# Optimization experiments

Measured on AMD Instinct MI355X. Metric: run time of the kernel, lower is better.

Reference implementation:

```python
import jax, jax.numpy as jnp
import numpy as np

DELTA_VAR = 0.5
DELTA_DIST = 1.5
LOSS_WEIGHT = 1.0
L_MAX = 17  # segment ids 0..16 (0 = background)
EPS = 1e-12


def setup_inputs() -> dict:
    key = jax.random.key(0)
    k1, k2 = jax.random.split(key)
    B, D, H, W = 16, 16, 288, 512
    emb = jax.random.normal(k1, (B, D, H, W), dtype=jnp.float32)
    seg = jax.random.randint(k2, (B, 1, H, W), 0, L_MAX, dtype=jnp.int64)
    return {"input": emb, "target": seg}


def _per_image_losses(e, s):
    # e: [D, N] float, s: [N] int labels in [0, L_MAX)
    D, N = e.shape
    et = e.T  # [N, D]
    cnt = jax.ops.segment_sum(jnp.ones((N,), e.dtype), s, num_segments=L_MAX)  # [L]
    sums = jax.ops.segment_sum(et, s, num_segments=L_MAX)                      # [L, D]
    present = (cnt > 0) & (jnp.arange(L_MAX) != 0)
    num_lanes = jnp.sum(present).astype(e.dtype)
    means = sums / jnp.maximum(cnt, 1.0)[:, None]                              # [L, D]

    # variance (pull) term: per-pixel distance to own-label centroid
    diff = et - means[s]                                                       # [N, D]
    nrm = jnp.sqrt(jnp.maximum(jnp.sum(diff * diff, axis=1), EPS))             # [N]
    term = jax.nn.relu(nrm - DELTA_VAR) ** 2
    per_label = jax.ops.segment_sum(term, s, num_segments=L_MAX) / jnp.maximum(cnt, 1.0)
    var_l = jnp.sum(jnp.where(present, per_label, 0.0)) / jnp.maximum(num_lanes, 1.0)
    var_l = jnp.where(num_lanes > 0, var_l, 0.0)

    # distance (push) term: pairwise centroid distances among present lanes
    d = means[:, None, :] - means[None, :, :]                                  # [L, L, D]
    sumsq = jnp.sum(d * d, axis=2)                                             # [L, L]
    pair_mask = present[:, None] & present[None, :] & ~jnp.eye(L_MAX, dtype=bool)
    dist = jnp.sqrt(jnp.where(pair_mask, sumsq, 1.0))
    push = jnp.sum(jnp.where(pair_mask, jax.nn.relu(DELTA_DIST - dist) ** 2, 0.0))
    denom = jnp.maximum(num_lanes * (num_lanes - 1.0), 1.0)
    dist_l = jnp.where(num_lanes > 1, push / denom / 2.0, 0.0)
    return var_l, dist_l


def reference(input, target):
    B, D, H, W = input.shape
    N = H * W
    emb = input.reshape(B, D, N)
    seg = target.reshape(B, N).astype(jnp.int32)
    var_l, dist_l = jax.vmap(_per_image_losses)(emb, seg)
    loss = (jnp.sum(var_l) + jnp.sum(dist_l)) / B
    return loss * LOSS_WEIGHT
```

## Files before the change

### kernel.cpp

```cpp
#include <hip/hip_runtime.h>

#define BB   16
#define DD   16
#define NN   (288*512)
#define LL   17
#define TPB  256
#define NREP 16

#define PB   48
#define QB   (NN/4/PB)
#define PBV  144

#define FSCALE 32768.0f
#define INV_FSCALE (1.0f/32768.0f)
#define MW_STRIDE 320


__global__ __launch_bounds__(TPB) void k_accum(const float* __restrict__ emb,
                                               const int* __restrict__ seg,
                                               int* __restrict__ part) {
    __shared__ int tab[NREP * 289];
    const int tid  = threadIdx.x;
    const int b    = blockIdx.y;
    const int blk  = blockIdx.x;
    const int dgrp = tid >> 6;
    const int j    = tid & 63;
    int* trep = tab + (j & (NREP - 1)) * 289;

    for (int i = tid; i < NREP * 289; i += TPB) tab[i] = 0;

    const float* embb = emb + (size_t)b * DD * NN;
    const int*   segb = seg + (size_t)b * NN;
    const float* r0 = embb + (size_t)(dgrp * 4 + 0) * NN;
    const float* r1 = embb + (size_t)(dgrp * 4 + 1) * NN;
    const float* r2 = embb + (size_t)(dgrp * 4 + 2) * NN;
    const float* r3 = embb + (size_t)(dgrp * 4 + 3) * NN;
    const int q0 = blk * QB;
    __syncthreads();

    int n = (q0 + j) * 4;
    int4   s4 = *(const int4*)(segb + n);
    float4 e0 = *(const float4*)(r0 + n);
    float4 e1 = *(const float4*)(r1 + n);
    float4 e2 = *(const float4*)(r2 + n);
    float4 e3 = *(const float4*)(r3 + n);

#pragma unroll
    for (int it = 0; it < QB / 64; ++it) {
        int4 s4n; float4 e0n, e1n, e2n, e3n;
        if (it + 1 < QB / 64) {
            const int nn_ = (q0 + (it + 1) * 64 + j) * 4;
            s4n = *(const int4*)(segb + nn_);
            e0n = *(const float4*)(r0 + nn_);
            e1n = *(const float4*)(r1 + nn_);
            e2n = *(const float4*)(r2 + nn_);
            e3n = *(const float4*)(r3 + nn_);
        }
        const int ch = dgrp * 4;
        if (s4.x) {
            const int o0 = s4.x * 17 + ch;
            atomicAdd(trep + o0 + 0, __float2int_rn(e0.x * FSCALE));
            atomicAdd(trep + o0 + 1, __float2int_rn(e1.x * FSCALE));
            atomicAdd(trep + o0 + 2, __float2int_rn(e2.x * FSCALE));
            atomicAdd(trep + o0 + 3, __float2int_rn(e3.x * FSCALE));
            if (dgrp == 0) atomicAdd(trep + s4.x * 17 + 16, 1);
        }
        if (s4.y) {
            const int o1 = s4.y * 17 + ch;
            atomicAdd(trep + o1 + 0, __float2int_rn(e0.y * FSCALE));
            atomicAdd(trep + o1 + 1, __float2int_rn(e1.y * FSCALE));
            atomicAdd(trep + o1 + 2, __float2int_rn(e2.y * FSCALE));
            atomicAdd(trep + o1 + 3, __float2int_rn(e3.y * FSCALE));
            if (dgrp == 0) atomicAdd(trep + s4.y * 17 + 16, 1);
        }
        if (s4.z) {
            const int o2 = s4.z * 17 + ch;
            atomicAdd(trep + o2 + 0, __float2int_rn(e0.z * FSCALE));
            atomicAdd(trep + o2 + 1, __float2int_rn(e1.z * FSCALE));
            atomicAdd(trep + o2 + 2, __float2int_rn(e2.z * FSCALE));
            atomicAdd(trep + o2 + 3, __float2int_rn(e3.z * FSCALE));
            if (dgrp == 0) atomicAdd(trep + s4.z * 17 + 16, 1);
        }
        if (s4.w) {
            const int o3 = s4.w * 17 + ch;
            atomicAdd(trep + o3 + 0, __float2int_rn(e0.w * FSCALE));
            atomicAdd(trep + o3 + 1, __float2int_rn(e1.w * FSCALE));
            atomicAdd(trep + o3 + 2, __float2int_rn(e2.w * FSCALE));
            atomicAdd(trep + o3 + 3, __float2int_rn(e3.w * FSCALE));
            if (dgrp == 0) atomicAdd(trep + s4.w * 17 + 16, 1);
        }
        s4 = s4n; e0 = e0n; e1 = e1n; e2 = e2n; e3 = e3n;
    }
    __syncthreads();

    int* pout = part + ((size_t)b * PB + blk) * 289;
    for (int i = tid; i < 289; i += TPB) {
        int v = 0;
#pragma unroll
        for (int r = 0; r < NREP; ++r) v += tab[r * 289 + i];
        pout[i] = v;
    }
}

__global__ __launch_bounds__(TPB) void k_reduce(const int* __restrict__ part,
                                                float* __restrict__ mw,
                                                float* __restrict__ vpart) {
    __shared__ float m[289];
    __shared__ float wl[17];
    __shared__ float psum[TPB / 64];
    const int tid = threadIdx.x;
    const int b = blockIdx.x;

    for (int i = tid; i < 289; i += TPB) {
        const int* p = part + (size_t)b * PB * 289 + i;
        int s = 0;
#pragma unroll 8
        for (int k = 0; k < PB; ++k) s += p[(size_t)k * 289];
        m[i] = (i % 17 == 16) ? (float)s : (float)s * INV_FSCALE;
    }
    __syncthreads();
    for (int i = tid; i < 272; i += TPB) {
        const int l = i >> 4, d = i & 15;
        m[l * 17 + d] /= fmaxf(m[l * 17 + 16], 1.f);
    }
    __syncthreads();

    int nl = 0;
#pragma unroll
    for (int l = 1; l < LL; ++l) nl += (m[l * 17 + 16] > 0.f) ? 1 : 0;
    const float nlf = (float)nl;
    if (tid < LL) {
        const bool pres = (tid != 0) && (m[tid * 17 + 16] > 0.f);
        wl[tid] = pres ? 1.f / (fmaxf(m[tid * 17 + 16], 1.f) * fmaxf(nlf, 1.f) * (float)BB)
                       : 0.f;
    }
    __syncthreads();

    float push = 0.f;
    if (nl > 1) {
        for (int p = tid; p < 289; p += TPB) {
            const int i = p / 17, jj = p % 17;
            if (i != jj && i > 0 && jj > 0 && m[i*17+16] > 0.f && m[jj*17+16] > 0.f) {
                float ss = 0.f;
#pragma unroll
                for (int d = 0; d < DD; ++d) {
                    const float df = m[i*17+d] - m[jj*17+d];
                    ss += df * df;
                }
                const float u = fmaxf(1.5f - sqrtf(ss), 0.f);
                push += u * u;
            }
        }
    }
#pragma unroll
    for (int off = 32; off; off >>= 1) push += __shfl_down(push, off, 64);
    if ((tid & 63) == 0) psum[tid >> 6] = push;
    __syncthreads();
    if (tid == 0) {
        const float tot = psum[0] + psum[1] + psum[2] + psum[3];
        vpart[(size_t)BB * PBV + b] =
            (nl > 1) ? tot / (fmaxf(nlf * (nlf - 1.f), 1.f) * 2.f * (float)BB) : 0.f;
    }

    for (int i = tid; i < 289 + LL; i += TPB)
        mw[(size_t)b * MW_STRIDE + i] = (i < 289) ? m[i] : wl[i - 289];
}

__global__ __launch_bounds__(TPB, 4) void k_var(const float* __restrict__ emb,
                                                const int* __restrict__ seg,
                                                const float* __restrict__ mw,
                                                float* __restrict__ vpart) {
    __shared__ float md[306];
    __shared__ float wsum[TPB / 64];
    const int tid = threadIdx.x;
    const int b = blockIdx.y;

    for (int i = tid; i < 306; i += TPB) md[i] = mw[(size_t)b * MW_STRIDE + i];
    __syncthreads();

    const float* embb = emb + (size_t)b * DD * NN;
    const int*   segb = seg + (size_t)b * NN;

    const int n = blockIdx.x * (TPB * 4) + tid * 4;
    const int4 s4 = *(const int4*)(segb + n);

    float4 e[DD];
#pragma unroll
    for (int d = 0; d < DD; ++d)
        e[d] = *(const float4*)(embb + (size_t)d * NN + n);

    const int o0 = s4.x * 17, o1 = s4.y * 17, o2 = s4.z * 17, o3 = s4.w * 17;
    float ss0 = 0.f, ss1 = 0.f, ss2 = 0.f, ss3 = 0.f;
#pragma unroll
    for (int d = 0; d < DD; ++d) {
        const float d0 = e[d].x - md[o0 + d]; ss0 += d0 * d0;
        const float d1 = e[d].y - md[o1 + d]; ss1 += d1 * d1;
        const float d2 = e[d].z - md[o2 + d]; ss2 += d2 * d2;
        const float d3 = e[d].w - md[o3 + d]; ss3 += d3 * d3;
    }
    float accl = 0.f, t;
    t = fmaxf(sqrtf(fmaxf(ss0, 1e-12f)) - 0.5f, 0.f); accl += t * t * md[289 + s4.x];
    t = fmaxf(sqrtf(fmaxf(ss1, 1e-12f)) - 0.5f, 0.f); accl += t * t * md[289 + s4.y];
    t = fmaxf(sqrtf(fmaxf(ss2, 1e-12f)) - 0.5f, 0.f); accl += t * t * md[289 + s4.z];
    t = fmaxf(sqrtf(fmaxf(ss3, 1e-12f)) - 0.5f, 0.f); accl += t * t * md[289 + s4.w];

#pragma unroll
    for (int off = 32; off; off >>= 1) accl += __shfl_down(accl, off, 64);
    if ((tid & 63) == 0) wsum[tid >> 6] = accl;
    __syncthreads();
    if (tid == 0)
        vpart[(size_t)b * PBV + blockIdx.x] = wsum[0] + wsum[1] + wsum[2] + wsum[3];
}

__global__ __launch_bounds__(TPB) void k_final(const float* __restrict__ vpart,
                                               float* __restrict__ out) {
    __shared__ float ws4[TPB / 64];
    float v = 0.f;
    for (int i = threadIdx.x; i < BB * PBV + BB; i += TPB) v += vpart[i];
#pragma unroll
    for (int off = 32; off; off >>= 1) v += __shfl_down(v, off, 64);
    if ((threadIdx.x & 63) == 0) ws4[threadIdx.x >> 6] = v;
    __syncthreads();
    if (threadIdx.x == 0) out[0] = ws4[0] + ws4[1] + ws4[2] + ws4[3];
}

extern "C" void kernel_launch(void* const* d_in, const int* in_sizes, int n_in,
                              void* d_out, int out_size, void* d_ws, size_t ws_size,
                              hipStream_t stream) {
    const float* emb = (const float*)d_in[0];
    const int*   seg = (const int*)d_in[1];
    float* out = (float*)d_out;

    int*   part  = (int*)d_ws;
    float* mw    = (float*)(part + (size_t)BB * PB * 289);
    float* vpart = mw + (size_t)BB * MW_STRIDE;

    k_accum <<<dim3(PB, BB), TPB, 0, stream>>>(emb, seg, part);
    k_reduce<<<BB, TPB, 0, stream>>>(part, mw, vpart);
    k_var   <<<dim3(PBV, BB), TPB, 0, stream>>>(emb, seg, mw, vpart);
    k_final <<<1, TPB, 0, stream>>>(vpart, out);
}
```

Baseline: 252.9 us.

## Fuse four kernels into one cooperative kernel with grid-wide syncs

Replaces the four-kernel pipeline (accumulate, reduce, variance, final) with a single cooperative launch that uses grid.sync between phases. The grid shrinks to 36x16 blocks so all 576 fit co-resident, and each block now covers four quads per thread in the variance phase. The aim is to remove launch gaps and kernel boundaries. The cost is grid-barrier overhead, fewer blocks in the accumulate phase, a serial reduce phase where only 16 blocks work while the rest wait, and lower occupancy from launch_bounds(256,3). If the cooperative launch fails, it falls back to separate kernels.

```diff
diff --git a/kernel.cpp b/kernel.cpp
--- a/kernel.cpp
+++ b/kernel.cpp
@@ -1,4 +1,7 @@
 #include <hip/hip_runtime.h>
+#include <hip/hip_cooperative_groups.h>
+
+namespace cg = cooperative_groups;
 
 #define BB   16
 #define DD   16
@@ -7,22 +10,20 @@
 #define TPB  256
 #define NREP 16
 
-#define PB   48
+#define PB   36
 #define QB   (NN/4/PB)
-#define PBV  144
 
 #define FSCALE 32768.0f
 #define INV_FSCALE (1.0f/32768.0f)
 #define MW_STRIDE 320
 
 
-__global__ __launch_bounds__(TPB) void k_accum(const float* __restrict__ emb,
-                                               const int* __restrict__ seg,
-                                               int* __restrict__ part) {
-    __shared__ int tab[NREP * 289];
+
+__device__ __forceinline__ void accum_body(const float* __restrict__ emb,
+                                           const int* __restrict__ seg,
+                                           int* __restrict__ part,
+                                           int* tab, int b, int sub) {
     const int tid  = threadIdx.x;
-    const int b    = blockIdx.y;
-    const int blk  = blockIdx.x;
     const int dgrp = tid >> 6;
     const int j    = tid & 63;
     int* trep = tab + (j & (NREP - 1)) * 289;
@@ -35,7 +36,7 @@
     const float* r1 = embb + (size_t)(dgrp * 4 + 1) * NN;
     const float* r2 = embb + (size_t)(dgrp * 4 + 2) * NN;
     const float* r3 = embb + (size_t)(dgrp * 4 + 3) * NN;
-    const int q0 = blk * QB;
+    const int q0 = sub * QB;
     __syncthreads();
 
     int n = (q0 + j) * 4;
@@ -47,7 +48,7 @@
 
 #pragma unroll
     for (int it = 0; it < QB / 64; ++it) {
-        int4 s4n; float4 e0n, e1n, e2n, e3n;
+        int4 s4n = s4; float4 e0n = e0, e1n = e1, e2n = e2, e3n = e3;
         if (it + 1 < QB / 64) {
             const int nn_ = (q0 + (it + 1) * 64 + j) * 4;
             s4n = *(const int4*)(segb + nn_);
@@ -93,7 +94,7 @@
     }
     __syncthreads();
 
-    int* pout = part + ((size_t)b * PB + blk) * 289;
+    int* pout = part + ((size_t)b * PB + sub) * 289;
     for (int i = tid; i < 289; i += TPB) {
         int v = 0;
 #pragma unroll
@@ -102,19 +103,17 @@
     }
 }
 
-__global__ __launch_bounds__(TPB) void k_reduce(const int* __restrict__ part,
-                                                float* __restrict__ mw,
-                                                float* __restrict__ vpart) {
-    __shared__ float m[289];
-    __shared__ float wl[17];
-    __shared__ float psum[TPB / 64];
+__device__ __forceinline__ void reduce_body(const int* __restrict__ part,
+                                            float* __restrict__ mw,
+                                            float* __restrict__ vpart,
+                                            float* m ,
+                                            float* wsum, int b) {
     const int tid = threadIdx.x;
-    const int b = blockIdx.x;
-
+    float* wl = m + 289;
     for (int i = tid; i < 289; i += TPB) {
         const int* p = part + (size_t)b * PB * 289 + i;
         int s = 0;
-#pragma unroll 8
+#pragma unroll 6
         for (int k = 0; k < PB; ++k) s += p[(size_t)k * 289];
         m[i] = (i % 17 == 16) ? (float)s : (float)s * INV_FSCALE;
     }
@@ -154,16 +153,114 @@
     }
 #pragma unroll
     for (int off = 32; off; off >>= 1) push += __shfl_down(push, off, 64);
-    if ((tid & 63) == 0) psum[tid >> 6] = push;
+    if ((tid & 63) == 0) wsum[tid >> 6] = push;
     __syncthreads();
     if (tid == 0) {
-        const float tot = psum[0] + psum[1] + psum[2] + psum[3];
-        vpart[(size_t)BB * PBV + b] =
+        const float tot = wsum[0] + wsum[1] + wsum[2] + wsum[3];
+        vpart[(size_t)BB * PB + b] =
             (nl > 1) ? tot / (fmaxf(nlf * (nlf - 1.f), 1.f) * 2.f * (float)BB) : 0.f;
     }
-
     for (int i = tid; i < 289 + LL; i += TPB)
         mw[(size_t)b * MW_STRIDE + i] = (i < 289) ? m[i] : wl[i - 289];
+}
+
+__device__ __forceinline__ void var_body(const float* __restrict__ emb,
+                                         const int* __restrict__ seg,
+                                         const float* __restrict__ mw,
+                                         float* __restrict__ vpart,
+                                         float* md ,
+                                         float* wsum, int b, int sub, int nquads) {
+    const int tid = threadIdx.x;
+    for (int i = tid; i < 306; i += TPB) md[i] = mw[(size_t)b * MW_STRIDE + i];
+    __syncthreads();
+
+    const float* embb = emb + (size_t)b * DD * NN;
+    const int*   segb = seg + (size_t)b * NN;
+    const int q0 = sub * QB;
+
+    float accl = 0.f;
+    for (int k = 0; k < nquads; ++k) {
+        const int nq = (q0 + k * 256 + tid) * 4;
+        const int4 sq = *(const int4*)(segb + nq);
+        float4 e[DD];
+#pragma unroll
+        for (int d = 0; d < DD; ++d)
+            e[d] = *(const float4*)(embb + (size_t)d * NN + nq);
+        const int o0 = sq.x * 17, o1 = sq.y * 17, o2 = sq.z * 17, o3 = sq.w * 17;
+        float ss0 = 0.f, ss1 = 0.f, ss2 = 0.f, ss3 = 0.f;
+#pragma unroll
+        for (int d = 0; d < DD; ++d) {
+            const float d0 = e[d].x - md[o0 + d]; ss0 += d0 * d0;
+            const float d1 = e[d].y - md[o1 + d]; ss1 += d1 * d1;
+            const float d2 = e[d].z - md[o2 + d]; ss2 += d2 * d2;
+            const float d3 = e[d].w - md[o3 + d]; ss3 += d3 * d3;
+        }
+        float t;
+        t = fmaxf(sqrtf(fmaxf(ss0, 1e-12f)) - 0.5f, 0.f); accl += t * t * md[289 + sq.x];
+        t = fmaxf(sqrtf(fmaxf(ss1, 1e-12f)) - 0.5f, 0.f); accl += t * t * md[289 + sq.y];
+        t = fmaxf(sqrtf(fmaxf(ss2, 1e-12f)) - 0.5f, 0.f); accl += t * t * md[289 + sq.z];
+        t = fmaxf(sqrtf(fmaxf(ss3, 1e-12f)) - 0.5f, 0.f); accl += t * t * md[289 + sq.w];
+    }
+#pragma unroll
+    for (int off = 32; off; off >>= 1) accl += __shfl_down(accl, off, 64);
+    if ((tid & 63) == 0) wsum[tid >> 6] = accl;
+    __syncthreads();
+    if (tid == 0)
+        vpart[(size_t)b * PB + sub] = wsum[0] + wsum[1] + wsum[2] + wsum[3];
+}
+
+__global__ __launch_bounds__(TPB, 3) void k_fused(const float* __restrict__ emb,
+                                                  const int* __restrict__ seg,
+                                                  int* __restrict__ part,
+                                                  float* __restrict__ mw,
+                                                  float* __restrict__ vpart,
+                                                  float* __restrict__ out) {
+    __shared__ int tab[NREP * 289];
+    __shared__ float wsum[TPB / 64];
+    cg::grid_group grid = cg::this_grid();
+
+    const int tid = threadIdx.x;
+    const int b   = blockIdx.y;
+    const int sub = blockIdx.x;
+
+    accum_body(emb, seg, part, tab, b, sub);
+    __threadfence();
+    grid.sync();
+
+    if (sub == 0) {
+        reduce_body(part, mw, vpart, (float*)tab, wsum, b);
+        __threadfence();
+    }
+    grid.sync();
+
+    var_body(emb, seg, mw, vpart, (float*)tab, wsum, b, sub, 4);
+    __threadfence();
+    grid.sync();
+
+    if (b == 0 && sub == 0) {
+        float v = 0.f;
+        for (int i = tid; i < BB * PB + BB; i += TPB) v += vpart[i];
+#pragma unroll
+        for (int off = 32; off; off >>= 1) v += __shfl_down(v, off, 64);
+        if ((tid & 63) == 0) wsum[tid >> 6] = v;
+        __syncthreads();
+        if (tid == 0) out[0] = wsum[0] + wsum[1] + wsum[2] + wsum[3];
+    }
+}
+
+__global__ __launch_bounds__(TPB) void k_accum(const float* __restrict__ emb,
+                                               const int* __restrict__ seg,
+                                               int* __restrict__ part) {
+    __shared__ int tab[NREP * 289];
+    accum_body(emb, seg, part, tab, blockIdx.y, blockIdx.x);
+}
+
+__global__ __launch_bounds__(TPB) void k_reduce(const int* __restrict__ part,
+                                                float* __restrict__ mw,
+                                                float* __restrict__ vpart) {
+    __shared__ float m[289 + 17];
+    __shared__ float wsum[TPB / 64];
+    reduce_body(part, mw, vpart, m, wsum, blockIdx.x);
 }
 
 __global__ __launch_bounds__(TPB, 4) void k_var(const float* __restrict__ emb,
@@ -172,51 +269,14 @@
                                                 float* __restrict__ vpart) {
     __shared__ float md[306];
     __shared__ float wsum[TPB / 64];
-    const int tid = threadIdx.x;
-    const int b = blockIdx.y;
-
-    for (int i = tid; i < 306; i += TPB) md[i] = mw[(size_t)b * MW_STRIDE + i];
-    __syncthreads();
-
-    const float* embb = emb + (size_t)b * DD * NN;
-    const int*   segb = seg + (size_t)b * NN;
-
-    const int n = blockIdx.x * (TPB * 4) + tid * 4;
-    const int4 s4 = *(const int4*)(segb + n);
-
-    float4 e[DD];
-#pragma unroll
-    for (int d = 0; d < DD; ++d)
-        e[d] = *(const float4*)(embb + (size_t)d * NN + n);
-
-    const int o0 = s4.x * 17, o1 = s4.y * 17, o2 = s4.z * 17, o3 = s4.w * 17;
-    float ss0 = 0.f, ss1 = 0.f, ss2 = 0.f, ss3 = 0.f;
-#pragma unroll
-    for (int d = 0; d < DD; ++d) {
-        const float d0 = e[d].x - md[o0 + d]; ss0 += d0 * d0;
-        const float d1 = e[d].y - md[o1 + d]; ss1 += d1 * d1;
-        const float d2 = e[d].z - md[o2 + d]; ss2 += d2 * d2;
-        const float d3 = e[d].w - md[o3 + d]; ss3 += d3 * d3;
-    }
-    float accl = 0.f, t;
-    t = fmaxf(sqrtf(fmaxf(ss0, 1e-12f)) - 0.5f, 0.f); accl += t * t * md[289 + s4.x];
-    t = fmaxf(sqrtf(fmaxf(ss1, 1e-12f)) - 0.5f, 0.f); accl += t * t * md[289 + s4.y];
-    t = fmaxf(sqrtf(fmaxf(ss2, 1e-12f)) - 0.5f, 0.f); accl += t * t * md[289 + s4.z];
-    t = fmaxf(sqrtf(fmaxf(ss3, 1e-12f)) - 0.5f, 0.f); accl += t * t * md[289 + s4.w];
-
-#pragma unroll
-    for (int off = 32; off; off >>= 1) accl += __shfl_down(accl, off, 64);
-    if ((tid & 63) == 0) wsum[tid >> 6] = accl;
-    __syncthreads();
-    if (tid == 0)
-        vpart[(size_t)b * PBV + blockIdx.x] = wsum[0] + wsum[1] + wsum[2] + wsum[3];
+    var_body(emb, seg, mw, vpart, md, wsum, blockIdx.y, blockIdx.x, 4);
 }
 
 __global__ __launch_bounds__(TPB) void k_final(const float* __restrict__ vpart,
                                                float* __restrict__ out) {
     __shared__ float ws4[TPB / 64];
     float v = 0.f;
-    for (int i = threadIdx.x; i < BB * PBV + BB; i += TPB) v += vpart[i];
+    for (int i = threadIdx.x; i < BB * PB + BB; i += TPB) v += vpart[i];
 #pragma unroll
     for (int off = 32; off; off >>= 1) v += __shfl_down(v, off, 64);
     if ((threadIdx.x & 63) == 0) ws4[threadIdx.x >> 6] = v;
@@ -235,8 +295,14 @@
     float* mw    = (float*)(part + (size_t)BB * PB * 289);
     float* vpart = mw + (size_t)BB * MW_STRIDE;
 
-    k_accum <<<dim3(PB, BB), TPB, 0, stream>>>(emb, seg, part);
-    k_reduce<<<BB, TPB, 0, stream>>>(part, mw, vpart);
-    k_var   <<<dim3(PBV, BB), TPB, 0, stream>>>(emb, seg, mw, vpart);
-    k_final <<<1, TPB, 0, stream>>>(vpart, out);
-}
+    void* args[] = {(void*)&emb, (void*)&seg, (void*)&part,
+                    (void*)&mw,  (void*)&vpart, (void*)&out};
+    hipError_t err = hipLaunchCooperativeKernel((void*)k_fused, dim3(PB, BB),
+                                                dim3(TPB), args, 0, stream);
+    if (err != hipSuccess) {
+        k_accum <<<dim3(PB, BB), TPB, 0, stream>>>(emb, seg, part);
+        k_reduce<<<BB, TPB, 0, stream>>>(part, mw, vpart);
+        k_var   <<<dim3(PB, BB), TPB, 0, stream>>>(emb, seg, mw, vpart);
+        k_final <<<1, TPB, 0, stream>>>(vpart, out);
+    }
+}
```

After: 582.2 us. +130.2%, slower.
